# Kernel tuning notes

Hardware: AMD Instinct MI355X
Metric: run time of the kernel (lower is better)

The kernel has to match this reference:

```python
import jax, jax.numpy as jnp
import numpy as np

B0 = 4
DIM = 128        # d_model / channels
D_INNER = 256    # expand * dim
D_STATE = 16
D_CONV = 4
DT_RANK = 8      # ceil(dim/16)
NSLICES = 16
IMG = (16, 24, 24)
EPS_LN = 1e-5    # nn.LayerNorm default
EPS_CF = 1e-6    # channels_first LayerNorm eps


def setup_inputs() -> dict:
    key = jax.random.key(0)
    ks = jax.random.split(key, 32)
    rn = lambda k, s, sc=1.0: jax.random.normal(k, s, jnp.float32) * sc
    inp = {"x": rn(ks[0], (B0, DIM) + IMG)}
    inp["ln_w"] = jnp.ones((DIM,), jnp.float32)
    inp["ln_b"] = jnp.zeros((DIM,), jnp.float32)
    inp["in_proj_w"] = rn(ks[1], (2 * D_INNER, DIM), 0.05)
    inp["out_proj_w"] = rn(ks[2], (DIM, D_INNER), 0.05)
    for i, sfx in enumerate(["f", "b", "s"]):
        b = 3 + i * 7
        inp[f"conv_w_{sfx}"] = rn(ks[b], (D_INNER, 1, D_CONV), 0.2)
        inp[f"conv_b_{sfx}"] = rn(ks[b + 1], (D_INNER,), 0.02)
        inp[f"xproj_w_{sfx}"] = rn(ks[b + 2], (DT_RANK + 2 * D_STATE, D_INNER), 0.05)
        inp[f"dtproj_w_{sfx}"] = rn(ks[b + 3], (D_INNER, DT_RANK), 0.1)
        inp[f"dtproj_b_{sfx}"] = rn(ks[b + 4], (D_INNER,), 0.1)
        # S4D-real-style init: A in [1, d_state]
        inp[f"A_log_{sfx}"] = jnp.log(jax.random.uniform(ks[b + 5], (D_INNER, D_STATE), jnp.float32, 1.0, 16.0))
        inp[f"D_{sfx}"] = jnp.ones((D_INNER,), jnp.float32)
    inp["nm_w"] = jnp.ones((DIM,), jnp.float32)
    inp["nm_b"] = jnp.zeros((DIM,), jnp.float32)
    return inp


def _mamba_inner(xz, conv_w, conv_b, xproj_w, dtproj_w, dtproj_b, A_log, Dp):
    """mamba_inner_fn_no_out_proj: xz (B, 2*d_inner, L) -> y (B, d_inner, L)."""
    d = conv_w.shape[0]
    x, z = xz[:, :d], xz[:, d:]
    # causal depthwise conv1d
    xc = jax.lax.conv_general_dilated(
        x, conv_w, (1,), [(conv_w.shape[-1] - 1, 0)],
        dimension_numbers=("NCH", "OIH", "NCH"), feature_group_count=d)
    xc = jax.nn.silu(xc + conv_b[None, :, None])
    x_dbl = jnp.einsum("bdl,rd->brl", xc, xproj_w)  # (B, R+2N, L)
    R = dtproj_w.shape[1]
    N = A_log.shape[1]
    dt = jax.nn.softplus(jnp.einsum("brl,dr->bdl", x_dbl[:, :R], dtproj_w) + dtproj_b[None, :, None])
    Bm, Cm = x_dbl[:, R:R + N], x_dbl[:, R + N:]
    A = -jnp.exp(A_log)  # (d, N)
    seq = (jnp.moveaxis(dt, -1, 0), jnp.moveaxis(xc, -1, 0),
           jnp.moveaxis(Bm, -1, 0), jnp.moveaxis(Cm, -1, 0))
    h0 = jnp.zeros((xz.shape[0], d, N), xz.dtype)

    def step(h, t):
        dt_t, u_t, B_t, C_t = t  # (B,d) (B,d) (B,N) (B,N)
        h = h * jnp.exp(dt_t[..., None] * A) + (dt_t * u_t)[..., None] * B_t[:, None, :]
        return h, jnp.einsum("bdn,bn->bd", h, C_t)

    _, ys = jax.lax.scan(step, h0, seq)  # ys: (L, B, d)
    y = jnp.moveaxis(ys, 0, -1) + Dp[None, :, None] * xc
    return y * jax.nn.silu(z)


def reference(x, ln_w, ln_b, in_proj_w, out_proj_w,
              conv_w_f, conv_b_f, xproj_w_f, dtproj_w_f, dtproj_b_f, A_log_f, D_f,
              conv_w_b, conv_b_b, xproj_w_b, dtproj_w_b, dtproj_b_b, A_log_b, D_b,
              conv_w_s, conv_b_s, xproj_w_s, dtproj_w_s, dtproj_b_s, A_log_s, D_s,
              nm_w, nm_b):
    B, C = x.shape[:2]
    img = x.shape[2:]
    L = int(np.prod(img))
    xf = jnp.transpose(x.reshape(B, C, L), (0, 2, 1))  # (B, L, C)
    # MambaLayer.norm (nn.LayerNorm over C)
    mu = xf.mean(-1, keepdims=True)
    var = ((xf - mu) ** 2).mean(-1, keepdims=True)
    xn = (xf - mu) / jnp.sqrt(var + EPS_LN) * ln_w + ln_b
    xz = jnp.einsum("blc,ec->bel", xn, in_proj_w)  # (B, 2*d_inner, L)
    # forward-direction scan
    out_f = _mamba_inner(xz, conv_w_f, conv_b_f, xproj_w_f, dtproj_w_f, dtproj_b_f, A_log_f, D_f)
    # backward-direction scan on flipped sequence, flipped back
    out_bw = jnp.flip(_mamba_inner(jnp.flip(xz, -1), conv_w_b, conv_b_b, xproj_w_b,
                                   dtproj_w_b, dtproj_b_b, A_log_b, D_b), -1)
    # slice-direction: torch chunk(nslices,-1) -> stack(-1) -> flatten(-2)
    ns, Lns = NSLICES, L // NSLICES
    xz_s = jnp.transpose(xz.reshape(B, 2 * D_INNER, ns, Lns), (0, 1, 3, 2)).reshape(B, 2 * D_INNER, L)
    out_s = _mamba_inner(xz_s, conv_w_s, conv_b_s, xproj_w_s, dtproj_w_s, dtproj_b_s, A_log_s, D_s)
    # torch: reshape(B,-1,ns,L//ns).permute(0,1,3,2).flatten(-2)
    out_s = jnp.transpose(out_s.reshape(B, D_INNER, ns, Lns), (0, 1, 3, 2)).reshape(B, D_INNER, L)
    y = jnp.einsum("bdl,cd->blc", out_f + out_bw + out_s, out_proj_w)  # out_proj, no bias
    x_mamba = jnp.transpose(y, (0, 2, 1)).reshape(x.shape) + x  # MambaLayer residual
    # SMBBlock: channels_first LayerNorm + residual
    mu2 = x_mamba.mean(1, keepdims=True)
    var2 = ((x_mamba - mu2) ** 2).mean(1, keepdims=True)
    bc = (C,) + (1,) * len(img)
    normed = nm_w.reshape(bc) * ((x_mamba - mu2) / jnp.sqrt(var2 + EPS_CF)) + nm_b.reshape(bc)
    return x_mamba + normed
```

## Files before the change

kernel.cpp:

```cpp
#include <hip/hip_runtime.h>

#define LSEQ 9216
#define CDIM 128
#define ED   512
#define DI   256
#define NST  16
#define LOG2E 1.44269504f
#define LN2  0.6931471805599453f

#if defined(__has_builtin)
#  if __has_builtin(__builtin_amdgcn_exp2f)
#    define FEXP2(x) __builtin_amdgcn_exp2f(x)
#  endif
#  if __has_builtin(__builtin_amdgcn_logf)
#    define FLOG2(x) __builtin_amdgcn_logf(x)
#  endif
#  if __has_builtin(__builtin_amdgcn_rcpf)
#    define FRCP(x) __builtin_amdgcn_rcpf(x)
#  endif
#endif
#ifndef FEXP2
#  define FEXP2(x) exp2f(x)
#endif
#ifndef FLOG2
#  define FLOG2(x) log2f(x)
#endif
#ifndef FRCP
#  define FRCP(x) (1.f / (x))
#endif

typedef __attribute__((ext_vector_type(8))) short short8v;
typedef __attribute__((ext_vector_type(4))) float float4v;

__device__ __forceinline__ float fsilu(float x) {
  return x * FRCP(1.f + FEXP2(-LOG2E * x));
}
__device__ __forceinline__ float fsoftplus(float x) {
  float sp = FLOG2(1.f + FEXP2(LOG2E * x)) * LN2;
  return (x > 20.f) ? x : sp;
}
__device__ __forceinline__ unsigned short f2bf(float f) {
  union { float f; unsigned u; } v; v.f = f;
  return (unsigned short)((v.u + 0x7FFFu + ((v.u >> 16) & 1u)) >> 16);
}
__device__ __forceinline__ int lmap(int p, int mode) {
  if (mode == 0) return p;
  if (mode == 1) return LSEQ - 1 - p;
  return (p & 15) * 576 + (p >> 4);
}

__global__ __launch_bounds__(256) void a2_kernel(
    const float* __restrict__ Af, const float* __restrict__ Ab,
    const float* __restrict__ As, float* __restrict__ A2) {
  int i = blockIdx.x * 256 + threadIdx.x;
  if (i >= 3 * DI * NST) return;
  int dir = i / (DI * NST), j = i % (DI * NST);
  const float* src = (dir == 0) ? Af : ((dir == 1) ? Ab : As);
  A2[i] = -expf(src[j]) * LOG2E;
}

__global__ __launch_bounds__(256) void wcast_kernel(
    const float* __restrict__ src, unsigned short* __restrict__ dst, int n) {
  int i = blockIdx.x * 256 + threadIdx.x;
  if (i < n) dst[i] = f2bf(src[i]);
}

__global__ __launch_bounds__(256) void ln_kernel(
    const float* __restrict__ x, const float* __restrict__ w,
    const float* __restrict__ bb, float* __restrict__ xn) {
  __shared__ float xt[CDIM][65];
  __shared__ float ps[4][64], pq[4][64];
  __shared__ float mu_s[64], rs_s[64];
  const int b = blockIdx.y, l0 = blockIdx.x * 64, tid = threadIdx.x;
  for (int idx = tid; idx < CDIM * 64; idx += 256) {
    int c = idx >> 6, ll = idx & 63;
    xt[c][ll] = x[((size_t)(b * CDIM + c)) * LSEQ + l0 + ll];
  }
  __syncthreads();
  {
    int ll = tid & 63, grp = tid >> 6;
    float s = 0.f, q = 0.f;
    for (int c = grp * 32; c < grp * 32 + 32; ++c) {
      float v = xt[c][ll]; s += v; q += v * v;
    }
    ps[grp][ll] = s; pq[grp][ll] = q;
  }
  __syncthreads();
  if (tid < 64) {
    float S = ps[0][tid] + ps[1][tid] + ps[2][tid] + ps[3][tid];
    float Q = pq[0][tid] + pq[1][tid] + pq[2][tid] + pq[3][tid];
    float mu = S * (1.f / 128.f);
    float var = Q * (1.f / 128.f) - mu * mu;
    mu_s[tid] = mu;
    rs_s[tid] = rsqrtf(var + 1e-5f);
  }
  __syncthreads();
  for (int idx = tid; idx < 64 * CDIM; idx += 256) {
    int c = idx & 127, ll = idx >> 7;
    float v = (xt[c][ll] - mu_s[ll]) * rs_s[ll] * w[c] + bb[c];
    xn[((size_t)(b * LSEQ + l0 + ll)) * CDIM + c] = v;
  }
}

__global__ __launch_bounds__(256) void gemm_mfma(
    const float* __restrict__ A, const unsigned short* __restrict__ Wb,
    float* __restrict__ Out, int N, int K, int ldo) {
  __shared__ __align__(16) unsigned short As[64][40];
  __shared__ __align__(16) unsigned short Bs[128][40];
  const int tid = threadIdx.x;
  const int lane = tid & 63, wid = tid >> 6;
  const int wr = wid >> 1, wc = wid & 1;
  const int m0 = blockIdx.x * 64, n0 = blockIdx.y * 128;
  float4v acc[2][4];
#pragma unroll
  for (int s = 0; s < 2; ++s)
#pragma unroll
    for (int t = 0; t < 4; ++t)
#pragma unroll
      for (int r = 0; r < 4; ++r) acc[s][t][r] = 0.f;

  const int srow = tid >> 2, sslot = tid & 3;
  for (int k0 = 0; k0 < K; k0 += 32) {
    {
      const float4* src = (const float4*)&A[(size_t)(m0 + srow) * K + k0 + sslot * 8];
      float4 f0 = src[0], f1 = src[1];
      short8v v;
      v[0] = (short)f2bf(f0.x); v[1] = (short)f2bf(f0.y);
      v[2] = (short)f2bf(f0.z); v[3] = (short)f2bf(f0.w);
      v[4] = (short)f2bf(f1.x); v[5] = (short)f2bf(f1.y);
      v[6] = (short)f2bf(f1.z); v[7] = (short)f2bf(f1.w);
      *(short8v*)&As[srow][sslot * 8] = v;
    }
#pragma unroll
    for (int i = 0; i < 2; ++i) {
      int row = i * 64 + srow;
      int n = n0 + row;
      short8v v;
      if (n < N) {
        v = *(const short8v*)&Wb[(size_t)n * K + k0 + sslot * 8];
      } else {
#pragma unroll
        for (int q = 0; q < 8; ++q) v[q] = 0;
      }
      *(short8v*)&Bs[row][sslot * 8] = v;
    }
    __syncthreads();
    const int kk = (lane >> 4) * 8;
    const int mr = wr * 32 + (lane & 15);
    const int nr = wc * 64 + (lane & 15);
    short8v a_frag[2], b_frag[4];
#pragma unroll
    for (int s = 0; s < 2; ++s)
      a_frag[s] = *(const short8v*)&As[mr + s * 16][kk];
#pragma unroll
    for (int t = 0; t < 4; ++t)
      b_frag[t] = *(const short8v*)&Bs[nr + t * 16][kk];
#pragma unroll
    for (int s = 0; s < 2; ++s)
#pragma unroll
      for (int t = 0; t < 4; ++t)
        acc[s][t] = __builtin_amdgcn_mfma_f32_16x16x32_bf16(
            a_frag[s], b_frag[t], acc[s][t], 0, 0, 0);
    __syncthreads();
  }
  const int rbase = (lane >> 4) * 4;
  const int cbase = lane & 15;
#pragma unroll
  for (int s = 0; s < 2; ++s)
#pragma unroll
    for (int t = 0; t < 4; ++t) {
      int n = n0 + wc * 64 + t * 16 + cbase;
      if (n < N) {
#pragma unroll
        for (int r = 0; r < 4; ++r) {
          int m = m0 + wr * 32 + s * 16 + rbase + r;
          Out[(size_t)m * ldo + n] = acc[s][t][r];
        }
      }
    }
}

template <int MODE>
__global__ __launch_bounds__(256) void conv_kernel(
    const float* __restrict__ xz, const float* __restrict__ cw,
    const float* __restrict__ cb, float* __restrict__ xc) {
  __shared__ float xs[67][64];
  const int p0 = blockIdx.x * 64, d0 = blockIdx.y * 64, b = blockIdx.z;
  const int tid = threadIdx.x;
  for (int idx = tid; idx < 67 * 64; idx += 256) {
    int pp = idx >> 6, dd = idx & 63;
    int q = p0 + pp - 3;
    float v = 0.f;
    if (q >= 0) {
      int l = lmap(q, MODE);
      v = xz[((size_t)b * LSEQ + l) * ED + d0 + dd];
    }
    xs[pp][dd] = v;
  }
  __syncthreads();
  const int dd = tid & 63, pg = tid >> 6;
  const int d = d0 + dd;
  const float w0 = cw[d * 4 + 0], w1 = cw[d * 4 + 1];
  const float w2 = cw[d * 4 + 2], w3 = cw[d * 4 + 3];
  const float bias = cb[d];
  for (int pp = pg * 16; pp < pg * 16 + 16; ++pp) {
    float acc = bias + w0 * xs[pp][dd] + w1 * xs[pp + 1][dd] +
                w2 * xs[pp + 2][dd] + w3 * xs[pp + 3][dd];
    xc[((size_t)b * LSEQ + p0 + pp) * DI + d] = fsilu(acc);
  }
}

template <int CHLT>
__global__ __launch_bounds__(256, 8) void scan_p1(
    const float* __restrict__ xc, const float* __restrict__ xdbl,
    const float* __restrict__ A2, const float* __restrict__ dtw,
    const float* __restrict__ dtbias, float* __restrict__ hout,
    float* __restrict__ dts) {
  __shared__ __align__(16) float Xl[CHLT][24];
  const int c = blockIdx.x, b = blockIdx.y, d = threadIdx.x;
  const int p0 = c * CHLT;
  for (int idx = d; idx < CHLT * 24; idx += 256) {
    int pr = idx / 24, r = idx % 24;
    Xl[pr][r] = xdbl[((size_t)b * LSEQ + p0 + pr) * 40 + r];
  }
  float a2[NST], h[NST], dw[8];
  {
    const float4* A2v = (const float4*)(A2 + d * NST);
#pragma unroll
    for (int q = 0; q < 4; ++q) {
      float4 t = A2v[q];
      a2[q * 4 + 0] = t.x; a2[q * 4 + 1] = t.y;
      a2[q * 4 + 2] = t.z; a2[q * 4 + 3] = t.w;
    }
    const float4* Wv = (const float4*)(dtw + d * 8);
    float4 w0 = Wv[0], w1 = Wv[1];
    dw[0] = w0.x; dw[1] = w0.y; dw[2] = w0.z; dw[3] = w0.w;
    dw[4] = w1.x; dw[5] = w1.y; dw[6] = w1.z; dw[7] = w1.w;
  }
#pragma unroll
  for (int n = 0; n < NST; ++n) h[n] = 0.f;
  const float dbias = dtbias[d];
  float dtsum = 0.f;
  const float* up = xc + ((size_t)b * LSEQ + p0) * DI + d;
  __syncthreads();
  for (int pr = 0; pr < CHLT; ++pr) {
    const float u = *up; up += DI;
    const float4* Xr = (const float4*)Xl[pr];
    float4 x0 = Xr[0], x1 = Xr[1];
    float raw = dbias;
    raw = fmaf(dw[0], x0.x, raw); raw = fmaf(dw[1], x0.y, raw);
    raw = fmaf(dw[2], x0.z, raw); raw = fmaf(dw[3], x0.w, raw);
    raw = fmaf(dw[4], x1.x, raw); raw = fmaf(dw[5], x1.y, raw);
    raw = fmaf(dw[6], x1.z, raw); raw = fmaf(dw[7], x1.w, raw);
    const float dtv = fsoftplus(raw);
    const float dtu = dtv * u;
    dtsum += dtv;
    float4 b0 = Xr[2], b1 = Xr[3], b2 = Xr[4], b3 = Xr[5];
    const float Bv[16] = {b0.x, b0.y, b0.z, b0.w, b1.x, b1.y, b1.z, b1.w,
                          b2.x, b2.y, b2.z, b2.w, b3.x, b3.y, b3.z, b3.w};
#pragma unroll
    for (int n = 0; n < NST; ++n) {
      float a = FEXP2(dtv * a2[n]);
      h[n] = fmaf(h[n], a, dtu * Bv[n]);
    }
  }
  float4* hb = (float4*)(hout + (((size_t)c * 4 + b) * DI + d) * NST);
#pragma unroll
  for (int q = 0; q < 4; ++q)
    hb[q] = make_float4(h[q * 4], h[q * 4 + 1], h[q * 4 + 2], h[q * 4 + 3]);
  dts[((size_t)c * 4 + b) * DI + d] = dtsum;
}

template <int SEG>
__global__ __launch_bounds__(256) void scan_p2a(
    float* __restrict__ hbuf, const float* __restrict__ dts,
    const float* __restrict__ A2, float* __restrict__ cumdts,
    float* __restrict__ segH, float* __restrict__ segdts) {
  const int s = blockIdx.x >> 4;
  const int rest = ((blockIdx.x & 15) << 8) + threadIdx.x;
  const int b = blockIdx.y;
  const int d = rest >> 4;
  const float a2 = A2[rest];
  const int c0 = s * SEG;
  float h = 0.f, cum = 0.f;
  float nh = hbuf[((size_t)(c0 * 4 + b) << 12) + rest];
  float nd = dts[(size_t)(c0 * 4 + b) * DI + d];
  for (int c = c0; c < c0 + SEG; ++c) {
    const float tmp = nh, dcur = nd;
    if (c + 1 < c0 + SEG) {
      nh = hbuf[((size_t)((c + 1) * 4 + b) << 12) + rest];
      nd = dts[(size_t)((c + 1) * 4 + b) * DI + d];
    }
    if ((rest & 15) == 0) cumdts[(size_t)(c * 4 + b) * DI + d] = cum;
    cum += dcur;
    hbuf[((size_t)(c * 4 + b) << 12) + rest] = h;
    h = fmaf(FEXP2(dcur * a2), h, tmp);
  }
  segH[((size_t)(s * 4 + b) << 12) + rest] = h;
  if ((rest & 15) == 0) segdts[(size_t)(s * 4 + b) * DI + d] = cum;
}

__global__ __launch_bounds__(256) void scan_p2b(
    const float* __restrict__ segH, const float* __restrict__ segdts,
    const float* __restrict__ A2, float* __restrict__ segcarry) {
  const int g = blockIdx.x * 256 + threadIdx.x;
  const int b = g >> 12;
  const int rest = g & 4095;
  const int d = rest >> 4;
  const float a2 = A2[rest];
  float carry = 0.f;
#pragma unroll
  for (int s = 0; s < 16; ++s) {
    segcarry[((size_t)(s * 4 + b) << 12) + rest] = carry;
    const float decay = FEXP2(segdts[(size_t)(s * 4 + b) * DI + d] * a2);
    carry = fmaf(decay, carry, segH[((size_t)(s * 4 + b) << 12) + rest]);
  }
}

template <int CHLT, int MODE>
__global__ __launch_bounds__(256, 8) void scan_p3(
    const float* __restrict__ xc, const float* __restrict__ xdbl,
    const float* __restrict__ xz, const float* __restrict__ A2,
    const float* __restrict__ dtw, const float* __restrict__ dtbias,
    const float* __restrict__ hinit, const float* __restrict__ cumdts,
    const float* __restrict__ segcarry, const float* __restrict__ Dp,
    float* __restrict__ yacc) {
  constexpr int SEG = (LSEQ / CHLT) / 16;
  __shared__ __align__(16) float Xl[CHLT][40];
  const int c = blockIdx.x, b = blockIdx.y, d = threadIdx.x;
  const int p0 = c * CHLT;
  for (int idx = d; idx < CHLT * 40; idx += 256) {
    int pr = idx / 40, r = idx % 40;
    Xl[pr][r] = xdbl[((size_t)b * LSEQ + p0 + pr) * 40 + r];
  }
  float a2[NST], h[NST], dw[8];
  {
    const float4* A2v = (const float4*)(A2 + d * NST);
    const float4* Hv = (const float4*)(hinit + (((size_t)c * 4 + b) * DI + d) * NST);
#pragma unroll
    for (int q = 0; q < 4; ++q) {
      float4 t = A2v[q], hh = Hv[q];
      a2[q * 4 + 0] = t.x; a2[q * 4 + 1] = t.y;
      a2[q * 4 + 2] = t.z; a2[q * 4 + 3] = t.w;
      h[q * 4 + 0] = hh.x; h[q * 4 + 1] = hh.y;
      h[q * 4 + 2] = hh.z; h[q * 4 + 3] = hh.w;
    }
    const float cum = cumdts[((size_t)c * 4 + b) * DI + d];
    const float4* SC = (const float4*)(segcarry +
        (((size_t)(c / SEG) * 4 + b) << 12) + d * NST);
#pragma unroll
    for (int q = 0; q < 4; ++q) {
      float4 sc = SC[q];
      const float scv[4] = {sc.x, sc.y, sc.z, sc.w};
#pragma unroll
      for (int r = 0; r < 4; ++r) {
        int n = q * 4 + r;
        h[n] = fmaf(FEXP2(a2[n] * cum), scv[r], h[n]);
      }
    }
    const float4* Wv = (const float4*)(dtw + d * 8);
    float4 w0 = Wv[0], w1 = Wv[1];
    dw[0] = w0.x; dw[1] = w0.y; dw[2] = w0.z; dw[3] = w0.w;
    dw[4] = w1.x; dw[5] = w1.y; dw[6] = w1.z; dw[7] = w1.w;
  }
  const float dbias = dtbias[d];
  const float Dv = Dp[d];

  const float* up = xc + ((size_t)b * LSEQ + p0) * DI + d;
  const float* zp;
  float* op;
  ptrdiff_t zstride, ostride;
  if (MODE == 0) {
    zp = xz + ((size_t)b * LSEQ + p0) * ED + DI + d;          zstride = ED;
    op = yacc + ((size_t)b * LSEQ + p0) * DI + d;             ostride = DI;
  } else if (MODE == 1) {
    zp = xz + ((size_t)b * LSEQ + (LSEQ - 1 - p0)) * ED + DI + d; zstride = -(ptrdiff_t)ED;
    op = yacc + ((size_t)b * LSEQ + (LSEQ - 1 - p0)) * DI + d;    ostride = -(ptrdiff_t)DI;
  } else {
    zp = nullptr; zstride = 0;
    const int lo0 = (p0 % 576) * 16 + p0 / 576;
    op = yacc + ((size_t)b * LSEQ + lo0) * DI + d;            ostride = 16 * DI;
  }
  __syncthreads();
  for (int pr = 0; pr < CHLT; ++pr) {
    const float u = *up; up += DI;
    const float4* Xr = (const float4*)Xl[pr];
    float4 x0 = Xr[0], x1 = Xr[1];
    float raw = dbias;
    raw = fmaf(dw[0], x0.x, raw); raw = fmaf(dw[1], x0.y, raw);
    raw = fmaf(dw[2], x0.z, raw); raw = fmaf(dw[3], x0.w, raw);
    raw = fmaf(dw[4], x1.x, raw); raw = fmaf(dw[5], x1.y, raw);
    raw = fmaf(dw[6], x1.z, raw); raw = fmaf(dw[7], x1.w, raw);
    const float dtv = fsoftplus(raw);
    const float dtu = dtv * u;
    float4 b0 = Xr[2], b1 = Xr[3], b2 = Xr[4], b3 = Xr[5];
    float4 c0 = Xr[6], c1 = Xr[7], c2 = Xr[8], c3 = Xr[9];
    const float Bv[16] = {b0.x, b0.y, b0.z, b0.w, b1.x, b1.y, b1.z, b1.w,
                          b2.x, b2.y, b2.z, b2.w, b3.x, b3.y, b3.z, b3.w};
    const float Cv[16] = {c0.x, c0.y, c0.z, c0.w, c1.x, c1.y, c1.z, c1.w,
                          c2.x, c2.y, c2.z, c2.w, c3.x, c3.y, c3.z, c3.w};
    float y0 = Dv * u, y1 = 0.f;
#pragma unroll
    for (int n = 0; n < NST; ++n) {
      float a = FEXP2(dtv * a2[n]);
      h[n] = fmaf(h[n], a, dtu * Bv[n]);
      if (n & 1) y1 = fmaf(h[n], Cv[n], y1);
      else       y0 = fmaf(h[n], Cv[n], y0);
    }
    float z;
    if (MODE == 2) {
      const int p = p0 + pr;
      const int lz = (p & 15) * 576 + (p >> 4);
      z = xz[((size_t)b * LSEQ + lz) * ED + DI + d];
    } else {
      z = *zp; zp += zstride;
    }
    const float val = (y0 + y1) * fsilu(z);
    if (MODE == 0) *op = val;
    else           *op += val;
    op += ostride;
  }
}

__global__ __launch_bounds__(256) void final_kernel(
    const float* __restrict__ x, const float* __restrict__ yout,
    const float* __restrict__ nmw, const float* __restrict__ nmb,
    float* __restrict__ out) {
  __shared__ float xt[CDIM][65];
  __shared__ float ps[4][64], pq[4][64];
  __shared__ float mu_s[64], rs_s[64];
  const int b = blockIdx.y, l0 = blockIdx.x * 64, tid = threadIdx.x;
  for (int idx = tid; idx < CDIM * 64; idx += 256) {
    int c = idx >> 6, ll = idx & 63;
    xt[c][ll] = x[((size_t)(b * CDIM + c)) * LSEQ + l0 + ll];
  }
  __syncthreads();
  for (int idx = tid; idx < 64 * CDIM; idx += 256) {
    int c = idx & 127, ll = idx >> 7;
    xt[c][ll] += yout[((size_t)(b * LSEQ + l0 + ll)) * CDIM + c];
  }
  __syncthreads();
  {
    int ll = tid & 63, grp = tid >> 6;
    float s = 0.f, q = 0.f;
    for (int c = grp * 32; c < grp * 32 + 32; ++c) {
      float v = xt[c][ll]; s += v; q += v * v;
    }
    ps[grp][ll] = s; pq[grp][ll] = q;
  }
  __syncthreads();
  if (tid < 64) {
    float S = ps[0][tid] + ps[1][tid] + ps[2][tid] + ps[3][tid];
    float Q = pq[0][tid] + pq[1][tid] + pq[2][tid] + pq[3][tid];
    float mu = S * (1.f / 128.f);
    float var = Q * (1.f / 128.f) - mu * mu;
    mu_s[tid] = mu;
    rs_s[tid] = rsqrtf(var + 1e-6f);
  }
  __syncthreads();
  for (int idx = tid; idx < CDIM * 64; idx += 256) {
    int c = idx >> 6, ll = idx & 63;
    float v = xt[c][ll];
    float nv = v + nmw[c] * (v - mu_s[ll]) * rs_s[ll] + nmb[c];
    out[((size_t)(b * CDIM + c)) * LSEQ + l0 + ll] = nv;
  }
}

extern "C" void kernel_launch(void* const* d_in, const int* in_sizes, int n_in,
                              void* d_out, int out_size, void* d_ws, size_t ws_size,
                              hipStream_t stream) {
  (void)in_sizes; (void)n_in; (void)out_size;
  const float* x         = (const float*)d_in[0];
  const float* ln_w      = (const float*)d_in[1];
  const float* ln_b      = (const float*)d_in[2];
  const float* in_proj_w = (const float*)d_in[3];
  const float* out_projw = (const float*)d_in[4];
  const float* conv_w[3] = {(const float*)d_in[5],  (const float*)d_in[12], (const float*)d_in[19]};
  const float* conv_b[3] = {(const float*)d_in[6],  (const float*)d_in[13], (const float*)d_in[20]};
  const float* xproj[3]  = {(const float*)d_in[7],  (const float*)d_in[14], (const float*)d_in[21]};
  const float* dtw[3]    = {(const float*)d_in[8],  (const float*)d_in[15], (const float*)d_in[22]};
  const float* dtb[3]    = {(const float*)d_in[9],  (const float*)d_in[16], (const float*)d_in[23]};
  const float* alog[3]   = {(const float*)d_in[10], (const float*)d_in[17], (const float*)d_in[24]};
  const float* Dvec[3]   = {(const float*)d_in[11], (const float*)d_in[18], (const float*)d_in[25]};
  const float* nm_w      = (const float*)d_in[26];
  const float* nm_b      = (const float*)d_in[27];

  float* ws    = (float*)d_ws;
  float* xn    = ws;
  float* xz    = ws + 4718592;
  float* xc    = ws + 23592960;
  float* xdbl  = ws + 33030144;
  float* yacc  = ws + 34504704;
  float* A2    = ws + 43941888;
  unsigned short* wb = (unsigned short*)(ws + 43954176);
  float* hout  = ws + 44019712;
  float* yout  = xn;

  int nch = 0;
  if      (ws_size >= (44019712ULL + 512 * 17408ULL) * 4) nch = 512;
  else if (ws_size >= (44019712ULL + 384 * 17408ULL) * 4) nch = 384;
  else if (ws_size >= (44019712ULL + 256 * 17408ULL) * 4) nch = 256;
  else if (ws_size >= (44019712ULL + 128 * 17408ULL) * 4) nch = 128;
  else return;
  float* dts      = hout + (size_t)nch * 16384;
  float* cumdts   = xn;
  float* segH     = xn + (size_t)nch * 1024;
  float* segdts   = segH + 262144;
  float* segcarry = segdts + 16384;

  unsigned short* wb_in  = wb;
  unsigned short* wb_xp0 = wb + 65536;
  unsigned short* wb_xp1 = wb + 75776;
  unsigned short* wb_xp2 = wb + 86016;
  unsigned short* wb_out = wb + 96256;
  unsigned short* wb_xp[3] = {wb_xp0, wb_xp1, wb_xp2};

  a2_kernel<<<48, 256, 0, stream>>>(alog[0], alog[1], alog[2], A2);
  wcast_kernel<<<256, 256, 0, stream>>>(in_proj_w, wb_in, 65536);
  wcast_kernel<<<40, 256, 0, stream>>>(xproj[0], wb_xp0, 10240);
  wcast_kernel<<<40, 256, 0, stream>>>(xproj[1], wb_xp1, 10240);
  wcast_kernel<<<40, 256, 0, stream>>>(xproj[2], wb_xp2, 10240);
  wcast_kernel<<<128, 256, 0, stream>>>(out_projw, wb_out, 32768);

  ln_kernel<<<dim3(LSEQ / 64, 4), 256, 0, stream>>>(x, ln_w, ln_b, xn);
  gemm_mfma<<<dim3(576, 4), 256, 0, stream>>>(xn, wb_in, xz, 512, 128, 512);

  for (int dir = 0; dir < 3; ++dir) {
    if (dir == 0)
      conv_kernel<0><<<dim3(LSEQ / 64, 4, 4), 256, 0, stream>>>(xz, conv_w[0], conv_b[0], xc);
    else if (dir == 1)
      conv_kernel<1><<<dim3(LSEQ / 64, 4, 4), 256, 0, stream>>>(xz, conv_w[1], conv_b[1], xc);
    else
      conv_kernel<2><<<dim3(LSEQ / 64, 4, 4), 256, 0, stream>>>(xz, conv_w[2], conv_b[2], xc);

    gemm_mfma<<<dim3(576, 1), 256, 0, stream>>>(xc, wb_xp[dir], xdbl, 40, 256, 40);

    const float* A2d = A2 + dir * 4096;
    dim3 sg(nch, 4);
    dim3 g2a(256, 4);
    if (nch == 512) {
      scan_p1<18><<<sg, 256, 0, stream>>>(xc, xdbl, A2d, dtw[dir], dtb[dir], hout, dts);
      scan_p2a<32><<<g2a, 256, 0, stream>>>(hout, dts, A2d, cumdts, segH, segdts);
    } else if (nch == 384) {
      scan_p1<24><<<sg, 256, 0, stream>>>(xc, xdbl, A2d, dtw[dir], dtb[dir], hout, dts);
      scan_p2a<24><<<g2a, 256, 0, stream>>>(hout, dts, A2d, cumdts, segH, segdts);
    } else if (nch == 256) {
      scan_p1<36><<<sg, 256, 0, stream>>>(xc, xdbl, A2d, dtw[dir], dtb[dir], hout, dts);
      scan_p2a<16><<<g2a, 256, 0, stream>>>(hout, dts, A2d, cumdts, segH, segdts);
    } else {
      scan_p1<72><<<sg, 256, 0, stream>>>(xc, xdbl, A2d, dtw[dir], dtb[dir], hout, dts);
      scan_p2a<8><<<g2a, 256, 0, stream>>>(hout, dts, A2d, cumdts, segH, segdts);
    }
    scan_p2b<<<64, 256, 0, stream>>>(segH, segdts, A2d, segcarry);

    if (nch == 512) {
      if (dir == 0)      scan_p3<18,0><<<sg,256,0,stream>>>(xc,xdbl,xz,A2d,dtw[0],dtb[0],hout,cumdts,segcarry,Dvec[0],yacc);
      else if (dir == 1) scan_p3<18,1><<<sg,256,0,stream>>>(xc,xdbl,xz,A2d,dtw[1],dtb[1],hout,cumdts,segcarry,Dvec[1],yacc);
      else               scan_p3<18,2><<<sg,256,0,stream>>>(xc,xdbl,xz,A2d,dtw[2],dtb[2],hout,cumdts,segcarry,Dvec[2],yacc);
    } else if (nch == 384) {
      if (dir == 0)      scan_p3<24,0><<<sg,256,0,stream>>>(xc,xdbl,xz,A2d,dtw[0],dtb[0],hout,cumdts,segcarry,Dvec[0],yacc);
      else if (dir == 1) scan_p3<24,1><<<sg,256,0,stream>>>(xc,xdbl,xz,A2d,dtw[1],dtb[1],hout,cumdts,segcarry,Dvec[1],yacc);
      else               scan_p3<24,2><<<sg,256,0,stream>>>(xc,xdbl,xz,A2d,dtw[2],dtb[2],hout,cumdts,segcarry,Dvec[2],yacc);
    } else if (nch == 256) {
      if (dir == 0)      scan_p3<36,0><<<sg,256,0,stream>>>(xc,xdbl,xz,A2d,dtw[0],dtb[0],hout,cumdts,segcarry,Dvec[0],yacc);
      else if (dir == 1) scan_p3<36,1><<<sg,256,0,stream>>>(xc,xdbl,xz,A2d,dtw[1],dtb[1],hout,cumdts,segcarry,Dvec[1],yacc);
      else               scan_p3<36,2><<<sg,256,0,stream>>>(xc,xdbl,xz,A2d,dtw[2],dtb[2],hout,cumdts,segcarry,Dvec[2],yacc);
    } else {
      if (dir == 0)      scan_p3<72,0><<<sg,256,0,stream>>>(xc,xdbl,xz,A2d,dtw[0],dtb[0],hout,cumdts,segcarry,Dvec[0],yacc);
      else if (dir == 1) scan_p3<72,1><<<sg,256,0,stream>>>(xc,xdbl,xz,A2d,dtw[1],dtb[1],hout,cumdts,segcarry,Dvec[1],yacc);
      else               scan_p3<72,2><<<sg,256,0,stream>>>(xc,xdbl,xz,A2d,dtw[2],dtb[2],hout,cumdts,segcarry,Dvec[2],yacc);
    }
  }
  gemm_mfma<<<dim3(576, 1), 256, 0, stream>>>(yacc, wb_out, yout, 128, 256, 128);
  final_kernel<<<dim3(LSEQ / 64, 4), 256, 0, stream>>>(x, yout, nm_w, nm_b, (float*)d_out);
}
```

Before: 504.8 us.

## Store intermediate activations and scan chunk states in bf16

Normalized input, in_proj output xz, conv output xc, and the per-chunk scan states are now stored as bf16 instead of fp32. GEMM kernels gain template flags to read bf16 A operands directly and write bf16 outputs. The aim is to roughly halve memory traffic in these bandwidth-bound stages. The workspace-size-dependent chunk count selection is replaced by a fixed layout with 512 chunks. The risk is extra rounding error in xz, xc and carried scan states, which could push accuracy past tolerance.

```diff
diff --git a/kernel.cpp b/kernel.cpp
--- a/kernel.cpp
+++ b/kernel.cpp
@@ -5,6 +5,9 @@
 #define ED   512
 #define DI   256
 #define NST  16
+#define NCH  512
+#define CHL  18
+#define SEG  32
 #define LOG2E 1.44269504f
 #define LN2  0.6931471805599453f
 
@@ -43,6 +46,10 @@
   union { float f; unsigned u; } v; v.f = f;
   return (unsigned short)((v.u + 0x7FFFu + ((v.u >> 16) & 1u)) >> 16);
 }
+__device__ __forceinline__ float bf2f(unsigned short u) {
+  union { unsigned u; float f; } v; v.u = ((unsigned)u) << 16;
+  return v.f;
+}
 __device__ __forceinline__ int lmap(int p, int mode) {
   if (mode == 0) return p;
   if (mode == 1) return LSEQ - 1 - p;
@@ -67,7 +74,7 @@
 
 __global__ __launch_bounds__(256) void ln_kernel(
     const float* __restrict__ x, const float* __restrict__ w,
-    const float* __restrict__ bb, float* __restrict__ xn) {
+    const float* __restrict__ bb, unsigned short* __restrict__ xn) {
   __shared__ float xt[CDIM][65];
   __shared__ float ps[4][64], pq[4][64];
   __shared__ float mu_s[64], rs_s[64];
@@ -98,13 +105,14 @@
   for (int idx = tid; idx < 64 * CDIM; idx += 256) {
     int c = idx & 127, ll = idx >> 7;
     float v = (xt[c][ll] - mu_s[ll]) * rs_s[ll] * w[c] + bb[c];
-    xn[((size_t)(b * LSEQ + l0 + ll)) * CDIM + c] = v;
-  }
-}
-
+    xn[((size_t)(b * LSEQ + l0 + ll)) * CDIM + c] = f2bf(v);
+  }
+}
+
+template <bool A_BF16, bool OUT_BF16>
 __global__ __launch_bounds__(256) void gemm_mfma(
-    const float* __restrict__ A, const unsigned short* __restrict__ Wb,
-    float* __restrict__ Out, int N, int K, int ldo) {
+    const void* __restrict__ Ap, const unsigned short* __restrict__ Wb,
+    void* __restrict__ Outp, int N, int K, int ldo) {
   __shared__ __align__(16) unsigned short As[64][40];
   __shared__ __align__(16) unsigned short Bs[128][40];
   const int tid = threadIdx.x;
@@ -121,7 +129,12 @@
 
   const int srow = tid >> 2, sslot = tid & 3;
   for (int k0 = 0; k0 < K; k0 += 32) {
-    {
+    if constexpr (A_BF16) {
+      const unsigned short* A = (const unsigned short*)Ap;
+      *(short8v*)&As[srow][sslot * 8] =
+          *(const short8v*)&A[(size_t)(m0 + srow) * K + k0 + sslot * 8];
+    } else {
+      const float* A = (const float*)Ap;
       const float4* src = (const float4*)&A[(size_t)(m0 + srow) * K + k0 + sslot * 8];
       float4 f0 = src[0], f1 = src[1];
       short8v v;
@@ -174,7 +187,10 @@
 #pragma unroll
         for (int r = 0; r < 4; ++r) {
           int m = m0 + wr * 32 + s * 16 + rbase + r;
-          Out[(size_t)m * ldo + n] = acc[s][t][r];
+          if constexpr (OUT_BF16)
+            ((unsigned short*)Outp)[(size_t)m * ldo + n] = f2bf(acc[s][t][r]);
+          else
+            ((float*)Outp)[(size_t)m * ldo + n] = acc[s][t][r];
         }
       }
     }
@@ -182,20 +198,25 @@
 
 template <int MODE>
 __global__ __launch_bounds__(256) void conv_kernel(
-    const float* __restrict__ xz, const float* __restrict__ cw,
-    const float* __restrict__ cb, float* __restrict__ xc) {
+    const unsigned short* __restrict__ xz, const float* __restrict__ cw,
+    const float* __restrict__ cb, unsigned short* __restrict__ xc) {
   __shared__ float xs[67][64];
   const int p0 = blockIdx.x * 64, d0 = blockIdx.y * 64, b = blockIdx.z;
   const int tid = threadIdx.x;
-  for (int idx = tid; idx < 67 * 64; idx += 256) {
-    int pp = idx >> 6, dd = idx & 63;
+  for (int idx = tid; idx < 67 * 32; idx += 256) {
+    int pp = idx >> 5, dd2 = idx & 31;
     int q = p0 + pp - 3;
-    float v = 0.f;
+    float v0 = 0.f, v1 = 0.f;
     if (q >= 0) {
       int l = lmap(q, MODE);
-      v = xz[((size_t)b * LSEQ + l) * ED + d0 + dd];
-    }
-    xs[pp][dd] = v;
+      unsigned uu = *(const unsigned*)&xz[((size_t)b * LSEQ + l) * ED + d0 + dd2 * 2];
+      union { unsigned u; float f; } a, c;
+      a.u = (uu & 0xFFFFu) << 16;
+      c.u = uu & 0xFFFF0000u;
+      v0 = a.f; v1 = c.f;
+    }
+    xs[pp][dd2 * 2] = v0;
+    xs[pp][dd2 * 2 + 1] = v1;
   }
   __syncthreads();
   const int dd = tid & 63, pg = tid >> 6;
@@ -206,20 +227,19 @@
   for (int pp = pg * 16; pp < pg * 16 + 16; ++pp) {
     float acc = bias + w0 * xs[pp][dd] + w1 * xs[pp + 1][dd] +
                 w2 * xs[pp + 2][dd] + w3 * xs[pp + 3][dd];
-    xc[((size_t)b * LSEQ + p0 + pp) * DI + d] = fsilu(acc);
-  }
-}
-
-template <int CHLT>
+    xc[((size_t)b * LSEQ + p0 + pp) * DI + d] = f2bf(fsilu(acc));
+  }
+}
+
 __global__ __launch_bounds__(256, 8) void scan_p1(
-    const float* __restrict__ xc, const float* __restrict__ xdbl,
+    const unsigned short* __restrict__ xc, const float* __restrict__ xdbl,
     const float* __restrict__ A2, const float* __restrict__ dtw,
-    const float* __restrict__ dtbias, float* __restrict__ hout,
+    const float* __restrict__ dtbias, unsigned short* __restrict__ hout,
     float* __restrict__ dts) {
-  __shared__ __align__(16) float Xl[CHLT][24];
+  __shared__ __align__(16) float Xl[CHL][24];
   const int c = blockIdx.x, b = blockIdx.y, d = threadIdx.x;
-  const int p0 = c * CHLT;
-  for (int idx = d; idx < CHLT * 24; idx += 256) {
+  const int p0 = c * CHL;
+  for (int idx = d; idx < CHL * 24; idx += 256) {
     int pr = idx / 24, r = idx % 24;
     Xl[pr][r] = xdbl[((size_t)b * LSEQ + p0 + pr) * 40 + r];
   }
@@ -241,10 +261,10 @@
   for (int n = 0; n < NST; ++n) h[n] = 0.f;
   const float dbias = dtbias[d];
   float dtsum = 0.f;
-  const float* up = xc + ((size_t)b * LSEQ + p0) * DI + d;
-  __syncthreads();
-  for (int pr = 0; pr < CHLT; ++pr) {
-    const float u = *up; up += DI;
+  const unsigned short* up = xc + ((size_t)b * LSEQ + p0) * DI + d;
+  __syncthreads();
+  for (int pr = 0; pr < CHL; ++pr) {
+    const float u = bf2f(*up); up += DI;
     const float4* Xr = (const float4*)Xl[pr];
     float4 x0 = Xr[0], x1 = Xr[1];
     float raw = dbias;
@@ -264,16 +284,23 @@
       h[n] = fmaf(h[n], a, dtu * Bv[n]);
     }
   }
-  float4* hb = (float4*)(hout + (((size_t)c * 4 + b) * DI + d) * NST);
-#pragma unroll
-  for (int q = 0; q < 4; ++q)
-    hb[q] = make_float4(h[q * 4], h[q * 4 + 1], h[q * 4 + 2], h[q * 4 + 3]);
+  unsigned short* hb = hout + (((size_t)c * 4 + b) * DI + d) * NST;
+  uint4 pk0, pk1;
+  pk0.x = ((unsigned)f2bf(h[1]) << 16) | f2bf(h[0]);
+  pk0.y = ((unsigned)f2bf(h[3]) << 16) | f2bf(h[2]);
+  pk0.z = ((unsigned)f2bf(h[5]) << 16) | f2bf(h[4]);
+  pk0.w = ((unsigned)f2bf(h[7]) << 16) | f2bf(h[6]);
+  pk1.x = ((unsigned)f2bf(h[9]) << 16) | f2bf(h[8]);
+  pk1.y = ((unsigned)f2bf(h[11]) << 16) | f2bf(h[10]);
+  pk1.z = ((unsigned)f2bf(h[13]) << 16) | f2bf(h[12]);
+  pk1.w = ((unsigned)f2bf(h[15]) << 16) | f2bf(h[14]);
+  *(uint4*)hb = pk0;
+  *(uint4*)(hb + 8) = pk1;
   dts[((size_t)c * 4 + b) * DI + d] = dtsum;
 }
 
-template <int SEG>
 __global__ __launch_bounds__(256) void scan_p2a(
-    float* __restrict__ hbuf, const float* __restrict__ dts,
+    unsigned short* __restrict__ hbuf, const float* __restrict__ dts,
     const float* __restrict__ A2, float* __restrict__ cumdts,
     float* __restrict__ segH, float* __restrict__ segdts) {
   const int s = blockIdx.x >> 4;
@@ -283,17 +310,17 @@
   const float a2 = A2[rest];
   const int c0 = s * SEG;
   float h = 0.f, cum = 0.f;
-  float nh = hbuf[((size_t)(c0 * 4 + b) << 12) + rest];
+  float nh = bf2f(hbuf[((size_t)(c0 * 4 + b) << 12) + rest]);
   float nd = dts[(size_t)(c0 * 4 + b) * DI + d];
   for (int c = c0; c < c0 + SEG; ++c) {
     const float tmp = nh, dcur = nd;
     if (c + 1 < c0 + SEG) {
-      nh = hbuf[((size_t)((c + 1) * 4 + b) << 12) + rest];
+      nh = bf2f(hbuf[((size_t)((c + 1) * 4 + b) << 12) + rest]);
       nd = dts[(size_t)((c + 1) * 4 + b) * DI + d];
     }
     if ((rest & 15) == 0) cumdts[(size_t)(c * 4 + b) * DI + d] = cum;
     cum += dcur;
-    hbuf[((size_t)(c * 4 + b) << 12) + rest] = h;
+    hbuf[((size_t)(c * 4 + b) << 12) + rest] = f2bf(h);
     h = fmaf(FEXP2(dcur * a2), h, tmp);
   }
   segH[((size_t)(s * 4 + b) << 12) + rest] = h;
@@ -317,33 +344,39 @@
   }
 }
 
-template <int CHLT, int MODE>
+template <int MODE>
 __global__ __launch_bounds__(256, 8) void scan_p3(
-    const float* __restrict__ xc, const float* __restrict__ xdbl,
-    const float* __restrict__ xz, const float* __restrict__ A2,
+    const unsigned short* __restrict__ xc, const float* __restrict__ xdbl,
+    const unsigned short* __restrict__ xz, const float* __restrict__ A2,
     const float* __restrict__ dtw, const float* __restrict__ dtbias,
-    const float* __restrict__ hinit, const float* __restrict__ cumdts,
+    const unsigned short* __restrict__ hinit, const float* __restrict__ cumdts,
     const float* __restrict__ segcarry, const float* __restrict__ Dp,
     float* __restrict__ yacc) {
-  constexpr int SEG = (LSEQ / CHLT) / 16;
-  __shared__ __align__(16) float Xl[CHLT][40];
+  __shared__ __align__(16) float Xl[CHL][40];
   const int c = blockIdx.x, b = blockIdx.y, d = threadIdx.x;
-  const int p0 = c * CHLT;
-  for (int idx = d; idx < CHLT * 40; idx += 256) {
+  const int p0 = c * CHL;
+  for (int idx = d; idx < CHL * 40; idx += 256) {
     int pr = idx / 40, r = idx % 40;
     Xl[pr][r] = xdbl[((size_t)b * LSEQ + p0 + pr) * 40 + r];
   }
   float a2[NST], h[NST], dw[8];
   {
     const float4* A2v = (const float4*)(A2 + d * NST);
-    const float4* Hv = (const float4*)(hinit + (((size_t)c * 4 + b) * DI + d) * NST);
 #pragma unroll
     for (int q = 0; q < 4; ++q) {
-      float4 t = A2v[q], hh = Hv[q];
+      float4 t = A2v[q];
       a2[q * 4 + 0] = t.x; a2[q * 4 + 1] = t.y;
       a2[q * 4 + 2] = t.z; a2[q * 4 + 3] = t.w;
-      h[q * 4 + 0] = hh.x; h[q * 4 + 1] = hh.y;
-      h[q * 4 + 2] = hh.z; h[q * 4 + 3] = hh.w;
+    }
+    const uint4* Hv = (const uint4*)(hinit + (((size_t)c * 4 + b) * DI + d) * NST);
+    uint4 pa = Hv[0], pb = Hv[1];
+    const unsigned pw[8] = {pa.x, pa.y, pa.z, pa.w, pb.x, pb.y, pb.z, pb.w};
+#pragma unroll
+    for (int j = 0; j < 8; ++j) {
+      union { unsigned u; float f; } lo, hi;
+      lo.u = (pw[j] & 0xFFFFu) << 16;
+      hi.u = pw[j] & 0xFFFF0000u;
+      h[2 * j] = lo.f; h[2 * j + 1] = hi.f;
     }
     const float cum = cumdts[((size_t)c * 4 + b) * DI + d];
     const float4* SC = (const float4*)(segcarry +
@@ -366,24 +399,24 @@
   const float dbias = dtbias[d];
   const float Dv = Dp[d];
 
-  const float* up = xc + ((size_t)b * LSEQ + p0) * DI + d;
-  const float* zp;
+  const unsigned short* up = xc + ((size_t)b * LSEQ + p0) * DI + d;
+  const unsigned short* zp;
   float* op;
   ptrdiff_t zstride, ostride;
   if (MODE == 0) {
-    zp = xz + ((size_t)b * LSEQ + p0) * ED + DI + d;          zstride = ED;
-    op = yacc + ((size_t)b * LSEQ + p0) * DI + d;             ostride = DI;
+    zp = xz + ((size_t)b * LSEQ + p0) * ED + DI + d;              zstride = ED;
+    op = yacc + ((size_t)b * LSEQ + p0) * DI + d;                 ostride = DI;
   } else if (MODE == 1) {
     zp = xz + ((size_t)b * LSEQ + (LSEQ - 1 - p0)) * ED + DI + d; zstride = -(ptrdiff_t)ED;
     op = yacc + ((size_t)b * LSEQ + (LSEQ - 1 - p0)) * DI + d;    ostride = -(ptrdiff_t)DI;
   } else {
     zp = nullptr; zstride = 0;
     const int lo0 = (p0 % 576) * 16 + p0 / 576;
-    op = yacc + ((size_t)b * LSEQ + lo0) * DI + d;            ostride = 16 * DI;
-  }
-  __syncthreads();
-  for (int pr = 0; pr < CHLT; ++pr) {
-    const float u = *up; up += DI;
+    op = yacc + ((size_t)b * LSEQ + lo0) * DI + d;                ostride = 16 * DI;
+  }
+  __syncthreads();
+  for (int pr = 0; pr < CHL; ++pr) {
+    const float u = bf2f(*up); up += DI;
     const float4* Xr = (const float4*)Xl[pr];
     float4 x0 = Xr[0], x1 = Xr[1];
     float raw = dbias;
@@ -411,9 +444,9 @@
     if (MODE == 2) {
       const int p = p0 + pr;
       const int lz = (p & 15) * 576 + (p >> 4);
-      z = xz[((size_t)b * LSEQ + lz) * ED + DI + d];
+      z = bf2f(xz[((size_t)b * LSEQ + lz) * ED + DI + d]);
     } else {
-      z = *zp; zp += zstride;
+      z = bf2f(*zp); zp += zstride;
     }
     const float val = (y0 + y1) * fsilu(z);
     if (MODE == 0) *op = val;
@@ -485,28 +518,22 @@
   const float* nm_w      = (const float*)d_in[26];
   const float* nm_b      = (const float*)d_in[27];
 
-  float* ws    = (float*)d_ws;
-  float* xn    = ws;
-  float* xz    = ws + 4718592;
-  float* xc    = ws + 23592960;
-  float* xdbl  = ws + 33030144;
-  float* yacc  = ws + 34504704;
-  float* A2    = ws + 43941888;
-  unsigned short* wb = (unsigned short*)(ws + 43954176);
-  float* hout  = ws + 44019712;
-  float* yout  = xn;
-
-  int nch = 0;
-  if      (ws_size >= (44019712ULL + 512 * 17408ULL) * 4) nch = 512;
-  else if (ws_size >= (44019712ULL + 384 * 17408ULL) * 4) nch = 384;
-  else if (ws_size >= (44019712ULL + 256 * 17408ULL) * 4) nch = 256;
-  else if (ws_size >= (44019712ULL + 128 * 17408ULL) * 4) nch = 128;
-  else return;
-  float* dts      = hout + (size_t)nch * 16384;
-  float* cumdts   = xn;
-  float* segH     = xn + (size_t)nch * 1024;
-  float* segdts   = segH + 262144;
-  float* segcarry = segdts + 16384;
+  float* ws = (float*)d_ws;
+  unsigned short* xn_us   = (unsigned short*)(ws);
+  unsigned short* xz_us   = (unsigned short*)(ws + 2359296);
+  unsigned short* xc_us   = (unsigned short*)(ws + 11796480);
+  float* xdbl   = ws + 16515072;
+  float* yacc   = ws + 17989632;
+  float* yout   = ws + 27426816;
+  float* A2     = ws + 32145408;
+  unsigned short* wb = (unsigned short*)(ws + 32157696);
+  unsigned short* hout_us = (unsigned short*)(ws + 32223232);
+  float* dts      = ws + 36417536;
+  float* cumdts   = ws + 36941824;
+  float* segH     = ws + 37466112;
+  float* segdts   = ws + 37728256;
+  float* segcarry = ws + 37744640;
+  if (ws_size < (size_t)38006784 * sizeof(float)) return;
 
   unsigned short* wb_in  = wb;
   unsigned short* wb_xp0 = wb + 65536;
@@ -522,55 +549,35 @@
   wcast_kernel<<<40, 256, 0, stream>>>(xproj[2], wb_xp2, 10240);
   wcast_kernel<<<128, 256, 0, stream>>>(out_projw, wb_out, 32768);
 
-  ln_kernel<<<dim3(LSEQ / 64, 4), 256, 0, stream>>>(x, ln_w, ln_b, xn);
-  gemm_mfma<<<dim3(576, 4), 256, 0, stream>>>(xn, wb_in, xz, 512, 128, 512);
+  ln_kernel<<<dim3(LSEQ / 64, 4), 256, 0, stream>>>(x, ln_w, ln_b, xn_us);
+  gemm_mfma<true, true><<<dim3(576, 4), 256, 0, stream>>>(xn_us, wb_in, xz_us, 512, 128, 512);
 
   for (int dir = 0; dir < 3; ++dir) {
     if (dir == 0)
-      conv_kernel<0><<<dim3(LSEQ / 64, 4, 4), 256, 0, stream>>>(xz, conv_w[0], conv_b[0], xc);
+      conv_kernel<0><<<dim3(LSEQ / 64, 4, 4), 256, 0, stream>>>(xz_us, conv_w[0], conv_b[0], xc_us);
     else if (dir == 1)
-      conv_kernel<1><<<dim3(LSEQ / 64, 4, 4), 256, 0, stream>>>(xz, conv_w[1], conv_b[1], xc);
+      conv_kernel<1><<<dim3(LSEQ / 64, 4, 4), 256, 0, stream>>>(xz_us, conv_w[1], conv_b[1], xc_us);
     else
-      conv_kernel<2><<<dim3(LSEQ / 64, 4, 4), 256, 0, stream>>>(xz, conv_w[2], conv_b[2], xc);
-
-    gemm_mfma<<<dim3(576, 1), 256, 0, stream>>>(xc, wb_xp[dir], xdbl, 40, 256, 40);
+      conv_kernel<2><<<dim3(LSEQ / 64, 4, 4), 256, 0, stream>>>(xz_us, conv_w[2], conv_b[2], xc_us);
+
+    gemm_mfma<true, false><<<dim3(576, 1), 256, 0, stream>>>(xc_us, wb_xp[dir], xdbl, 40, 256, 40);
 
     const float* A2d = A2 + dir * 4096;
-    dim3 sg(nch, 4);
-    dim3 g2a(256, 4);
-    if (nch == 512) {
-      scan_p1<18><<<sg, 256, 0, stream>>>(xc, xdbl, A2d, dtw[dir], dtb[dir], hout, dts);
-      scan_p2a<32><<<g2a, 256, 0, stream>>>(hout, dts, A2d, cumdts, segH, segdts);
-    } else if (nch == 384) {
-      scan_p1<24><<<sg, 256, 0, stream>>>(xc, xdbl, A2d, dtw[dir], dtb[dir], hout, dts);
-      scan_p2a<24><<<g2a, 256, 0, stream>>>(hout, dts, A2d, cumdts, segH, segdts);
-    } else if (nch == 256) {
-      scan_p1<36><<<sg, 256, 0, stream>>>(xc, xdbl, A2d, dtw[dir], dtb[dir], hout, dts);
-      scan_p2a<16><<<g2a, 256, 0, stream>>>(hout, dts, A2d, cumdts, segH, segdts);
-    } else {
-      scan_p1<72><<<sg, 256, 0, stream>>>(xc, xdbl, A2d, dtw[dir], dtb[dir], hout, dts);
-      scan_p2a<8><<<g2a, 256, 0, stream>>>(hout, dts, A2d, cumdts, segH, segdts);
-    }
+    dim3 sg(NCH, 4);
+    scan_p1<<<sg, 256, 0, stream>>>(xc_us, xdbl, A2d, dtw[dir], dtb[dir], hout_us, dts);
+    scan_p2a<<<dim3(256, 4), 256, 0, stream>>>(hout_us, dts, A2d, cumdts, segH, segdts);
     scan_p2b<<<64, 256, 0, stream>>>(segH, segdts, A2d, segcarry);
 
-    if (nch == 512) {
-      if (dir == 0)      scan_p3<18,0><<<sg,256,0,stream>>>(xc,xdbl,xz,A2d,dtw[0],dtb[0],hout,cumdts,segcarry,Dvec[0],yacc);
-      else if (dir == 1) scan_p3<18,1><<<sg,256,0,stream>>>(xc,xdbl,xz,A2d,dtw[1],dtb[1],hout,cumdts,segcarry,Dvec[1],yacc);
-      else               scan_p3<18,2><<<sg,256,0,stream>>>(xc,xdbl,xz,A2d,dtw[2],dtb[2],hout,cumdts,segcarry,Dvec[2],yacc);
-    } else if (nch == 384) {
-      if (dir == 0)      scan_p3<24,0><<<sg,256,0,stream>>>(xc,xdbl,xz,A2d,dtw[0],dtb[0],hout,cumdts,segcarry,Dvec[0],yacc);
-      else if (dir == 1) scan_p3<24,1><<<sg,256,0,stream>>>(xc,xdbl,xz,A2d,dtw[1],dtb[1],hout,cumdts,segcarry,Dvec[1],yacc);
-      else               scan_p3<24,2><<<sg,256,0,stream>>>(xc,xdbl,xz,A2d,dtw[2],dtb[2],hout,cumdts,segcarry,Dvec[2],yacc);
-    } else if (nch == 256) {
-      if (dir == 0)      scan_p3<36,0><<<sg,256,0,stream>>>(xc,xdbl,xz,A2d,dtw[0],dtb[0],hout,cumdts,segcarry,Dvec[0],yacc);
-      else if (dir == 1) scan_p3<36,1><<<sg,256,0,stream>>>(xc,xdbl,xz,A2d,dtw[1],dtb[1],hout,cumdts,segcarry,Dvec[1],yacc);
-      else               scan_p3<36,2><<<sg,256,0,stream>>>(xc,xdbl,xz,A2d,dtw[2],dtb[2],hout,cumdts,segcarry,Dvec[2],yacc);
-    } else {
-      if (dir == 0)      scan_p3<72,0><<<sg,256,0,stream>>>(xc,xdbl,xz,A2d,dtw[0],dtb[0],hout,cumdts,segcarry,Dvec[0],yacc);
-      else if (dir == 1) scan_p3<72,1><<<sg,256,0,stream>>>(xc,xdbl,xz,A2d,dtw[1],dtb[1],hout,cumdts,segcarry,Dvec[1],yacc);
-      else               scan_p3<72,2><<<sg,256,0,stream>>>(xc,xdbl,xz,A2d,dtw[2],dtb[2],hout,cumdts,segcarry,Dvec[2],yacc);
-    }
-  }
-  gemm_mfma<<<dim3(576, 1), 256, 0, stream>>>(yacc, wb_out, yout, 128, 256, 128);
+    if (dir == 0)
+      scan_p3<0><<<sg, 256, 0, stream>>>(xc_us, xdbl, xz_us, A2d, dtw[0], dtb[0],
+                                         hout_us, cumdts, segcarry, Dvec[0], yacc);
+    else if (dir == 1)
+      scan_p3<1><<<sg, 256, 0, stream>>>(xc_us, xdbl, xz_us, A2d, dtw[1], dtb[1],
+                                         hout_us, cumdts, segcarry, Dvec[1], yacc);
+    else
+      scan_p3<2><<<sg, 256, 0, stream>>>(xc_us, xdbl, xz_us, A2d, dtw[2], dtb[2],
+                                         hout_us, cumdts, segcarry, Dvec[2], yacc);
+  }
+  gemm_mfma<false, false><<<dim3(576, 1), 256, 0, stream>>>(yacc, wb_out, yout, 128, 256, 128);
   final_kernel<<<dim3(LSEQ / 64, 4), 256, 0, stream>>>(x, yout, nm_w, nm_b, (float*)d_out);
 }
```

New measurement: 481.7 us. 4.6% less time.
